# Kernel tuning notes

Measured on AMD Instinct MI355X. Metric: run time of the kernel, lower is better.

## Reference

```python
import jax, jax.numpy as jnp
import numpy as np

B, S, D, H = 4, 2048, 1024, 16
E = D // H  # head_size = 64


def setup_inputs() -> dict:
    key = jax.random.key(0)
    ks = jax.random.split(key, 6)
    scale = 1.0 / np.sqrt(D)
    embedded = jax.random.normal(ks[0], (B, S, D), dtype=jnp.float32)
    # Per-head Q/K/V projection weights, stacked over heads: [H, D, E]
    Wq = jax.random.normal(ks[1], (H, D, E), dtype=jnp.float32) * scale
    Wk = jax.random.normal(ks[2], (H, D, E), dtype=jnp.float32) * scale
    Wv = jax.random.normal(ks[3], (H, D, E), dtype=jnp.float32) * scale
    # Output projection (nn.Linear(model_dim, model_dim))
    Wo = jax.random.normal(ks[4], (D, D), dtype=jnp.float32) * scale
    bo = jax.random.normal(ks[5], (D,), dtype=jnp.float32) * scale
    return {"embedded": embedded, "Wq": Wq, "Wk": Wk, "Wv": Wv, "Wo": Wo, "bo": bo}


def reference(embedded, Wq, Wk, Wv, Wo, bo):
    # Batched over heads instead of the original Python loop; same math.
    q = jnp.einsum('bsd,hde->bhse', embedded, Wq)  # [B,H,S,E]
    k = jnp.einsum('bsd,hde->bhse', embedded, Wk)
    v = jnp.einsum('bsd,hde->bhse', embedded, Wv)
    scores = jnp.einsum('bhse,bhte->bhst', q, k) / jnp.sqrt(jnp.float32(E))
    causal = jnp.tril(jnp.ones((S, S), dtype=bool))  # [S,S]
    scores = jnp.where(causal, scores, jnp.float32(-jnp.inf))
    attn = jax.nn.softmax(scores, axis=-1)  # [B,H,S,S]
    out = jnp.einsum('bhst,bhte->bhse', attn, v)  # [B,H,S,E]
    # concat heads along last dim: [B,S,H*E] == [B,S,D]
    out = out.transpose(0, 2, 1, 3).reshape(B, S, D)
    # output projection (dropout is identity in eval mode)
    return out @ Wo.T + bo
```

## Files before the change

kernel.cpp:

```cpp
#include <hip/hip_runtime.h>
#include <hip/hip_bf16.h>

#define B_ 4
#define S_ 2048
#define D_ 1024
#define H_ 16
#define E_ 64
#define M_ (B_*S_)
#define NQKV_ 3072

typedef __attribute__((ext_vector_type(8))) short bf16x8;
typedef __attribute__((ext_vector_type(4))) float f32x4;
typedef __attribute__((ext_vector_type(16))) float f32x16;
typedef __attribute__((ext_vector_type(4))) unsigned short u16x4;
typedef unsigned short u16;

#define QSCALE 0.18033688011f
#define AS1 __attribute__((address_space(1)))
#define AS3 __attribute__((address_space(3)))

static __device__ __forceinline__ u16 f2bf(float f) {
  unsigned u = __builtin_bit_cast(unsigned, f);
  unsigned r = (u + 0x7FFFu + ((u >> 16) & 1u)) >> 16;
  return (u16)r;
}

static __device__ __forceinline__ unsigned pk2(float a, float b) {
  unsigned r;
  asm("v_cvt_pk_bf16_f32 %0, %1, %2" : "=v"(r) : "v"(a), "v"(b));
  return r;
}


__global__ __launch_bounds__(256) void cvt4(const float* __restrict__ in,
                                            u16* __restrict__ out, int n4) {
  int i = blockIdx.x * 256 + threadIdx.x;
  if (i >= n4) return;
  f32x4 v = ((const f32x4*)in)[i];
  u16x4 o;
  o.x = f2bf(v.x); o.y = f2bf(v.y); o.z = f2bf(v.z); o.w = f2bf(v.w);
  ((u16x4*)out)[i] = o;
}

__global__ __launch_bounds__(256) void cvt_wqkv(const float* __restrict__ Wq,
                                                const float* __restrict__ Wk,
                                                const float* __restrict__ Wv,
                                                u16* __restrict__ Wt) {
  __shared__ float t[64][65];
  const int h = blockIdx.x >> 4;
  const int db = (blockIdx.x & 15) * 64;
  const int tid = threadIdx.x;
  const float* srcs[3] = {Wq, Wk, Wv};
#pragma unroll
  for (int m = 0; m < 3; ++m) {
    const float* src = srcs[m] + (size_t)h * 65536 + (size_t)db * 64;
    __syncthreads();
#pragma unroll
    for (int i = 0; i < 16; ++i) {
      int idx = i * 256 + tid;
      int d = idx >> 6, e = idx & 63;
      t[e][d] = src[d * 64 + e];
    }
    __syncthreads();
    u16* dst = Wt + (size_t)(m * 1024 + h * 64) * 1024 + db;
#pragma unroll
    for (int i = 0; i < 16; ++i) {
      int idx = i * 256 + tid;
      int e = idx >> 6, d = idx & 63;
      dst[(size_t)e * 1024 + d] = f2bf(t[e][d]);
    }
  }
}


template<bool FP32OUT>
__global__ __launch_bounds__(256) void gemm_bt(const u16* __restrict__ A,
                                               const u16* __restrict__ Bt,
                                               void* __restrict__ Cv, int ldC,
                                               u16* __restrict__ Vt,
                                               const float* __restrict__ bias,
                                               int M, int N, int K) {
  __shared__ u16 As[128 * 32];
  __shared__ u16 Bs[128 * 32];
  const int tid = threadIdx.x;
  const int lane = tid & 63, wid = tid >> 6;
  const int bm = blockIdx.x, bn = blockIdx.y;
  const int wr = wid >> 1, wc = wid & 1;
  const int ll = lane & 15, lg = lane >> 4;

  f32x4 acc[4][4] = {};

  const int srow = lane >> 2;
  const int scol = (lane & 3) * 8;

  for (int k0 = 0; k0 < K; k0 += 32) {
#pragma unroll
    for (int p = 0; p < 2; ++p) {
      int row = p * 64 + wid * 16 + srow;
      const u16* ga = A + (size_t)(bm * 128 + row) * K + k0 + scol;
      __builtin_amdgcn_global_load_lds(
          (const AS1 void*)ga, (AS3 void*)(As + p * 2048 + wid * 512), 16, 0, 0);
      const u16* gb = Bt + (size_t)(bn * 128 + row) * K + k0 + scol;
      __builtin_amdgcn_global_load_lds(
          (const AS1 void*)gb, (AS3 void*)(Bs + p * 2048 + wid * 512), 16, 0, 0);
    }
    __syncthreads();
    bf16x8 af[4], bfr[4];
#pragma unroll
    for (int mi = 0; mi < 4; ++mi)
      af[mi] = *(const bf16x8*)&As[(wr * 64 + mi * 16 + ll) * 32 + lg * 8];
#pragma unroll
    for (int ni = 0; ni < 4; ++ni)
      bfr[ni] = *(const bf16x8*)&Bs[(wc * 64 + ni * 16 + ll) * 32 + lg * 8];
#pragma unroll
    for (int mi = 0; mi < 4; ++mi)
#pragma unroll
      for (int ni = 0; ni < 4; ++ni)
        acc[mi][ni] = __builtin_amdgcn_mfma_f32_16x16x32_bf16(af[mi], bfr[ni],
                                                              acc[mi][ni], 0, 0, 0);
    __syncthreads();
  }

  const int crow0 = bm * 128 + wr * 64;
  const int ccol0 = bn * 128 + wc * 64 + ll;
  const bool vblk = (Vt != nullptr) && (bn >= 16);
  const float qs = (Vt != nullptr && bn < 8) ? QSCALE : 1.0f;
  const int sig = (((lg & 1) << 1) | (lg >> 1)) << 2;
#pragma unroll
  for (int mi = 0; mi < 4; ++mi) {
#pragma unroll
    for (int ni = 0; ni < 4; ++ni) {
      int c = ccol0 + ni * 16;
      if (vblk) {
        int r0 = crow0 + mi * 16 + lg * 4;
        int bb = r0 >> 11, s0 = r0 & 2047;
        int s0p = (s0 & ~15) | sig;
        u16x4 pkv;
        pkv.x = f2bf(acc[mi][ni][0]); pkv.y = f2bf(acc[mi][ni][1]);
        pkv.z = f2bf(acc[mi][ni][2]); pkv.w = f2bf(acc[mi][ni][3]);
        *(u16x4*)&Vt[((size_t)(bb * 1024 + (c - 2048))) * 2048 + s0p] = pkv;
      } else {
#pragma unroll
        for (int j = 0; j < 4; ++j) {
          int r = crow0 + mi * 16 + lg * 4 + j;
          if (FP32OUT) {
            ((float*)Cv)[(size_t)r * ldC + c] = acc[mi][ni][j] + bias[c];
          } else {
            ((u16*)Cv)[(size_t)r * ldC + c] = f2bf(acc[mi][ni][j] * qs);
          }
        }
      }
    }
  }
}


#define SWZ(r) ((((r) & 7) ^ ((((r) >> 3) & 3) << 1)) << 4)

__global__ __launch_bounds__(512, 2) void attn(const u16* __restrict__ QK,
                                               const u16* __restrict__ Vt,
                                               u16* __restrict__ AO) {
  __shared__ u16 Klds[4][4096];
  __shared__ u16 Vlds[4][4096];

  const int wg = blockIdx.x;
  const int lin = (wg & 7) * 32 + (wg >> 3);
  const int bh = lin >> 2, pr = lin & 3;
  const int b = bh >> 4, h = bh & 15;
  const int tid = threadIdx.x;
  const int lane = tid & 63, wv = tid >> 6;
  const int lq = lane & 31, hi = lane >> 5;

  const int srow = tid >> 3;
  const int scolb = ((tid & 7) * 16) ^ SWZ(srow);
  const char* ksrc = (const char*)(QK + (size_t)(b * S_ + srow) * 2048 + 1024 + h * E_) + scolb;
  const char* vsrc = (const char*)(Vt + (size_t)(bh * 64 + srow) * 2048) + scolb;

  const int nktA = 4 * pr + 4;
  const int NS = 36;

  auto stage = [&](int sq, int kb) {
    char* kd = (char*)&Klds[0][0] + (sq & 3) * 8192 + wv * 1024;
    char* vd = (char*)&Vlds[0][0] + (sq & 3) * 8192 + wv * 1024;
    __builtin_amdgcn_global_load_lds((const AS1 void*)(ksrc + (size_t)kb * 4096),
                                     (AS3 void*)kd, 16, 0, 0);
    __builtin_amdgcn_global_load_lds((const AS1 void*)(vsrc + kb * 2),
                                     (AS3 void*)vd, 16, 0, 0);
  };

  stage(0, 0);
  stage(1, (1 < nktA ? 1 : 1 - nktA) * 64);

  int seq = 0;
  for (int ph = 0; ph < 2; ++ph) {
    const int qt = ph ? 7 - pr : pr;
    const int nkt = 4 * qt + 4;
    const int qw0 = qt * 256 + wv * 32;
    const int q = qw0 + lq;

    const u16* qp = QK + (size_t)(b * S_ + q) * 2048 + h * E_;
    bf16x8 qf[4];
#pragma unroll
    for (int c = 0; c < 4; ++c)
      qf[c] = *(const bf16x8*)(qp + c * 16 + hi * 8);

    float m_run = -INFINITY, l_part = 0.f;
    f32x16 o0 = {}, o1 = {};

    for (int kt = 0; kt < nkt; ++kt, ++seq) {
      if (seq + 2 < NS) {
        int s2 = seq + 2;
        stage(s2, (s2 < nktA ? s2 : s2 - nktA) * 64);
      }
      if (seq < NS - 2)       asm volatile("s_waitcnt vmcnt(4)" ::: "memory");
      else if (seq == NS - 2) asm volatile("s_waitcnt vmcnt(2)" ::: "memory");
      else                    asm volatile("s_waitcnt vmcnt(0)" ::: "memory");
      __builtin_amdgcn_s_barrier();

      const int kb = kt * 64;
      if (kb > qw0 + 31) continue;
      const char* kbuf = (const char*)&Klds[0][0] + (seq & 3) * 8192;
      const char* vbuf = (const char*)&Vlds[0][0] + (seq & 3) * 8192;

      auto half = [&](int kb2) __attribute__((always_inline)) {
        f32x16 sc = {};
        __builtin_amdgcn_s_setprio(1);
        const int krow = kb2 * 32 + lq;
#pragma unroll
        for (int c = 0; c < 4; ++c) {
          bf16x8 kf = *(const bf16x8*)(kbuf + krow * 128 +
                                       ((c * 32 + hi * 16) ^ SWZ(krow)));
          sc = __builtin_amdgcn_mfma_f32_32x32x16_bf16(kf, qf[c], sc, 0, 0, 0);
        }
        __builtin_amdgcn_s_setprio(0);

        if (kb + kb2 * 32 + 31 > qw0) {
#pragma unroll
          for (int r = 0; r < 16; ++r) {
            int key = kb + kb2 * 32 + (r & 3) + 8 * (r >> 2) + 4 * hi;
            if (key > q) sc[r] = -1e30f;
          }
        }

        float pm = sc[0];
#pragma unroll
        for (int r = 1; r < 16; ++r) pm = fmaxf(pm, sc[r]);
        if (__any(pm - m_run > 8.0f)) {
          float g = fmaxf(pm, __shfl_xor(pm, 32, 64));
          float mn = fmaxf(m_run, g);
          float corr = exp2f(m_run - mn);
          m_run = mn;
          l_part *= corr;
          o0 *= corr;
          o1 *= corr;
        }

        float p[16];
#pragma unroll
        for (int r = 0; r < 16; ++r) {
          p[r] = exp2f(sc[r] - m_run);
          l_part += p[r];
        }
        __builtin_amdgcn_s_setprio(1);
#pragma unroll
        for (int gg = 0; gg < 2; ++gg) {
          union { unsigned w[4]; bf16x8 v; } pf;
          pf.w[0] = pk2(p[gg * 8 + 0], p[gg * 8 + 1]);
          pf.w[1] = pk2(p[gg * 8 + 2], p[gg * 8 + 3]);
          pf.w[2] = pk2(p[gg * 8 + 4], p[gg * 8 + 5]);
          pf.w[3] = pk2(p[gg * 8 + 6], p[gg * 8 + 7]);
          const int g = kb2 * 2 + gg;
          {
            bf16x8 vf = *(const bf16x8*)(vbuf + lq * 128 +
                                         ((g * 32 + hi * 16) ^ SWZ(lq)));
            o0 = __builtin_amdgcn_mfma_f32_32x32x16_bf16(vf, pf.v, o0, 0, 0, 0);
          }
          {
            const int er = 32 + lq;
            bf16x8 vf = *(const bf16x8*)(vbuf + er * 128 +
                                         ((g * 32 + hi * 16) ^ SWZ(er)));
            o1 = __builtin_amdgcn_mfma_f32_32x32x16_bf16(vf, pf.v, o1, 0, 0, 0);
          }
        }
        __builtin_amdgcn_s_setprio(0);
      };

      half(0);
      if (kb + 32 <= qw0 + 31) half(1);
    }

    float l = l_part + __shfl_xor(l_part, 32, 64);
    float rl = 1.0f / l;

#pragma unroll
    for (int qd = 0; qd < 4; ++qd) {
      u16x4 w0, w1;
#pragma unroll
      for (int j = 0; j < 4; ++j) {
        w0[j] = f2bf(o0[qd * 4 + j] * rl);
        w1[j] = f2bf(o1[qd * 4 + j] * rl);
      }
      const size_t base = (size_t)(b * S_ + q) * D_ + h * E_ + 8 * qd + 4 * hi;
      *(u16x4*)&AO[base] = w0;
      *(u16x4*)&AO[base + 32] = w1;
    }
  }
}


extern "C" void kernel_launch(void* const* d_in, const int* in_sizes, int n_in,
                              void* d_out, int out_size, void* d_ws, size_t ws_size,
                              hipStream_t stream) {
  const float* embedded = (const float*)d_in[0];
  const float* Wq = (const float*)d_in[1];
  const float* Wk = (const float*)d_in[2];
  const float* Wv = (const float*)d_in[3];
  const float* Wo = (const float*)d_in[4];
  const float* bo = (const float*)d_in[5];
  float* out = (float*)d_out;

  char* ws = (char*)d_ws;
  u16* X    = (u16*)(ws);
  u16* Wqkv = (u16*)(ws + (16u << 20));
  u16* WoT  = (u16*)(ws + (22u << 20));
  u16* QK   = (u16*)(ws + (24u << 20));
  u16* Vt   = (u16*)(ws + (56u << 20));
  u16* AO   = (u16*)(ws + (72u << 20));

  cvt4<<<8192, 256, 0, stream>>>(embedded, X, 2097152);
  cvt_wqkv<<<256, 256, 0, stream>>>(Wq, Wk, Wv, Wqkv);
  cvt4<<<1024, 256, 0, stream>>>(Wo, WoT, 262144);
  gemm_bt<false><<<dim3(64, 24), 256, 0, stream>>>(X, Wqkv, QK, 2048, Vt,
                                                   nullptr, M_, NQKV_, 1024);
  attn<<<256, 512, 0, stream>>>(QK, Vt, AO);
  gemm_bt<true><<<dim3(64, 8), 256, 0, stream>>>(AO, WoT, out, 1024, nullptr,
                                                 bo, M_, 1024, 1024);
}
```

Baseline: 187.7 us.

## Add dedicated double-buffered QKV GEMM with async global-to-LDS loads

Replaces the generic 128x128 bf16 GEMM for the fused QKV projection with a dedicated 256x192-tile kernel using 512 threads, K-step 64, and double-buffered LDS filled by global_load_lds with an XOR swizzle. The next K-tile is prefetched while the MFMA loop runs, and s_setprio raises priority around the math. This targets the global-load latency exposed by the old single-buffered loop and the low data reuse of its smaller tiles. The cost is far more LDS per block (one block per CU) and a grid of 512 blocks, which may leave load imbalance across CUs.

```diff
diff --git a/kernel.cpp b/kernel.cpp
--- a/kernel.cpp
+++ b/kernel.cpp
@@ -18,6 +18,8 @@
 #define QSCALE 0.18033688011f
 #define AS1 __attribute__((address_space(1)))
 #define AS3 __attribute__((address_space(3)))
+
+#define SWZ(r) ((((r) & 7) ^ ((((r) >> 3) & 3) << 1)) << 4)
 
 static __device__ __forceinline__ u16 f2bf(float f) {
   unsigned u = __builtin_bit_cast(unsigned, f);
@@ -68,6 +70,111 @@
       int idx = i * 256 + tid;
       int e = idx >> 6, d = idx & 63;
       dst[(size_t)e * 1024 + d] = f2bf(t[e][d]);
+    }
+  }
+}
+
+
+__global__ __launch_bounds__(512, 1) void gemm_qkv(const u16* __restrict__ A,
+                                                   const u16* __restrict__ Bt,
+                                                   u16* __restrict__ QK,
+                                                   u16* __restrict__ Vt) {
+  __shared__ u16 As[2][256 * 64];
+  __shared__ u16 Bs[2][192 * 64];
+  const int tid = threadIdx.x;
+  const int lane = tid & 63, wv = tid >> 6;
+  const int ll = lane & 15, lg = lane >> 4;
+  const int wm = wv >> 2, wn = wv & 3;
+  const int bm = blockIdx.x, bn = blockIdx.y;
+
+  const int sr = tid >> 3;
+  const int scb = (tid & 7) * 16;
+  const char* asrc[4];
+  const char* bsrc[3];
+#pragma unroll
+  for (int i = 0; i < 4; ++i) {
+    int row = i * 64 + sr;
+    asrc[i] = (const char*)(A + (size_t)(bm * 256 + row) * 1024) + (scb ^ SWZ(row));
+  }
+#pragma unroll
+  for (int i = 0; i < 3; ++i) {
+    int row = i * 64 + sr;
+    bsrc[i] = (const char*)(Bt + (size_t)(bn * 192 + row) * 1024) + (scb ^ SWZ(row));
+  }
+
+  auto stage = [&](int t) {
+    const size_t adv = (size_t)t * 128;
+    char* ad = (char*)&As[t & 1][0] + tid * 16;
+    char* bd = (char*)&Bs[t & 1][0] + tid * 16;
+#pragma unroll
+    for (int i = 0; i < 4; ++i)
+      __builtin_amdgcn_global_load_lds((const AS1 void*)(asrc[i] + adv),
+                                       (AS3 void*)(ad + i * 8192), 16, 0, 0);
+#pragma unroll
+    for (int i = 0; i < 3; ++i)
+      __builtin_amdgcn_global_load_lds((const AS1 void*)(bsrc[i] + adv),
+                                       (AS3 void*)(bd + i * 8192), 16, 0, 0);
+  };
+
+  f32x4 acc[8][3] = {};
+
+  stage(0);
+  for (int t = 0; t < 16; ++t) {
+    if (t + 1 < 16) stage(t + 1);
+    if (t < 15) asm volatile("s_waitcnt vmcnt(7)" ::: "memory");
+    else        asm volatile("s_waitcnt vmcnt(0)" ::: "memory");
+    __builtin_amdgcn_s_barrier();
+
+    const char* ab = (const char*)&As[t & 1][0];
+    const char* bb = (const char*)&Bs[t & 1][0];
+
+    bf16x8 bf_[3][2];
+#pragma unroll
+    for (int ni = 0; ni < 3; ++ni) {
+      int row = wn * 48 + ni * 16 + ll;
+#pragma unroll
+      for (int ks = 0; ks < 2; ++ks)
+        bf_[ni][ks] = *(const bf16x8*)(bb + row * 128 +
+                                       ((ks * 64 + lg * 16) ^ SWZ(row)));
+    }
+    __builtin_amdgcn_s_setprio(1);
+#pragma unroll
+    for (int mi = 0; mi < 8; ++mi) {
+      int row = wm * 128 + mi * 16 + ll;
+#pragma unroll
+      for (int ks = 0; ks < 2; ++ks) {
+        bf16x8 af = *(const bf16x8*)(ab + row * 128 +
+                                     ((ks * 64 + lg * 16) ^ SWZ(row)));
+#pragma unroll
+        for (int ni = 0; ni < 3; ++ni)
+          acc[mi][ni] = __builtin_amdgcn_mfma_f32_16x16x32_bf16(
+              af, bf_[ni][ks], acc[mi][ni], 0, 0, 0);
+      }
+    }
+    __builtin_amdgcn_s_setprio(0);
+    __builtin_amdgcn_s_barrier();
+  }
+
+  const int sig = (((lg & 1) << 1) | (lg >> 1)) << 2;
+#pragma unroll
+  for (int mi = 0; mi < 8; ++mi) {
+#pragma unroll
+    for (int ni = 0; ni < 3; ++ni) {
+      int c = bn * 192 + wn * 48 + ni * 16 + ll;
+      int r0 = bm * 256 + wm * 128 + mi * 16 + lg * 4;
+      if (c >= 2048) {
+        int bb2 = r0 >> 11, s0 = r0 & 2047;
+        int s0p = (s0 & ~15) | sig;
+        u16x4 pkv;
+        pkv.x = f2bf(acc[mi][ni][0]); pkv.y = f2bf(acc[mi][ni][1]);
+        pkv.z = f2bf(acc[mi][ni][2]); pkv.w = f2bf(acc[mi][ni][3]);
+        *(u16x4*)&Vt[((size_t)(bb2 * 1024 + (c - 2048))) * 2048 + s0p] = pkv;
+      } else {
+        const float qs = (c < 1024) ? QSCALE : 1.0f;
+#pragma unroll
+        for (int j = 0; j < 4; ++j)
+          QK[(size_t)(r0 + j) * 2048 + c] = f2bf(acc[mi][ni][j] * qs);
+      }
     }
   }
 }
@@ -123,39 +230,24 @@
 
   const int crow0 = bm * 128 + wr * 64;
   const int ccol0 = bn * 128 + wc * 64 + ll;
-  const bool vblk = (Vt != nullptr) && (bn >= 16);
-  const float qs = (Vt != nullptr && bn < 8) ? QSCALE : 1.0f;
-  const int sig = (((lg & 1) << 1) | (lg >> 1)) << 2;
 #pragma unroll
   for (int mi = 0; mi < 4; ++mi) {
 #pragma unroll
     for (int ni = 0; ni < 4; ++ni) {
       int c = ccol0 + ni * 16;
-      if (vblk) {
-        int r0 = crow0 + mi * 16 + lg * 4;
-        int bb = r0 >> 11, s0 = r0 & 2047;
-        int s0p = (s0 & ~15) | sig;
-        u16x4 pkv;
-        pkv.x = f2bf(acc[mi][ni][0]); pkv.y = f2bf(acc[mi][ni][1]);
-        pkv.z = f2bf(acc[mi][ni][2]); pkv.w = f2bf(acc[mi][ni][3]);
-        *(u16x4*)&Vt[((size_t)(bb * 1024 + (c - 2048))) * 2048 + s0p] = pkv;
-      } else {
-#pragma unroll
-        for (int j = 0; j < 4; ++j) {
-          int r = crow0 + mi * 16 + lg * 4 + j;
-          if (FP32OUT) {
-            ((float*)Cv)[(size_t)r * ldC + c] = acc[mi][ni][j] + bias[c];
-          } else {
-            ((u16*)Cv)[(size_t)r * ldC + c] = f2bf(acc[mi][ni][j] * qs);
-          }
+#pragma unroll
+      for (int j = 0; j < 4; ++j) {
+        int r = crow0 + mi * 16 + lg * 4 + j;
+        if (FP32OUT) {
+          ((float*)Cv)[(size_t)r * ldC + c] = acc[mi][ni][j] + bias[c];
+        } else {
+          ((u16*)Cv)[(size_t)r * ldC + c] = f2bf(acc[mi][ni][j]);
         }
       }
     }
   }
 }
 
-
-#define SWZ(r) ((((r) & 7) ^ ((((r) >> 3) & 3) << 1)) << 4)
 
 __global__ __launch_bounds__(512, 2) void attn(const u16* __restrict__ QK,
                                                const u16* __restrict__ Vt,
@@ -330,8 +422,7 @@
   cvt4<<<8192, 256, 0, stream>>>(embedded, X, 2097152);
   cvt_wqkv<<<256, 256, 0, stream>>>(Wq, Wk, Wv, Wqkv);
   cvt4<<<1024, 256, 0, stream>>>(Wo, WoT, 262144);
-  gemm_bt<false><<<dim3(64, 24), 256, 0, stream>>>(X, Wqkv, QK, 2048, Vt,
-                                                   nullptr, M_, NQKV_, 1024);
+  gemm_qkv<<<dim3(32, 16), 512, 0, stream>>>(X, Wqkv, QK, Vt);
   attn<<<256, 512, 0, stream>>>(QK, Vt, AO);
   gemm_bt<true><<<dim3(64, 8), 256, 0, stream>>>(AO, WoT, out, 1024, nullptr,
                                                  bo, M_, 1024, 1024);
```

Result: faster. 179.9 us (-4.2%).

## Fuse conversion kernels and rewrite GEMMs with larger tiles and triple-buffered LDS pipeline

Applied to the files above, without the earlier changes.

The three fp32-to-bf16 conversion launches are merged into one kernel that dispatches on block index. Both projection GEMMs are rewritten as 512-thread kernels with larger tiles (256x384 for QKV, 256x128 for the output). They use a three-stage global-to-LDS prefetch with explicit vmcnt waits and raised scheduling priority around the MFMA loop. The goal is to cut launch overhead and hide global load latency behind compute. The cost is more LDS and registers per block and fewer blocks (256 per GEMM), which can hurt occupancy and load balance.

```diff
diff --git a/kernel.cpp b/kernel.cpp
--- a/kernel.cpp
+++ b/kernel.cpp
@@ -19,6 +19,8 @@
 #define AS1 __attribute__((address_space(1)))
 #define AS3 __attribute__((address_space(3)))
 
+#define SWZ(r) ((((r) & 7) ^ ((((r) >> 3) & 3) << 1)) << 4)
+
 static __device__ __forceinline__ u16 f2bf(float f) {
   unsigned u = __builtin_bit_cast(unsigned, f);
   unsigned r = (u + 0x7FFFu + ((u >> 16) & 1u)) >> 16;
@@ -32,130 +34,232 @@
 }
 
 
-__global__ __launch_bounds__(256) void cvt4(const float* __restrict__ in,
-                                            u16* __restrict__ out, int n4) {
-  int i = blockIdx.x * 256 + threadIdx.x;
-  if (i >= n4) return;
-  f32x4 v = ((const f32x4*)in)[i];
-  u16x4 o;
-  o.x = f2bf(v.x); o.y = f2bf(v.y); o.z = f2bf(v.z); o.w = f2bf(v.w);
-  ((u16x4*)out)[i] = o;
-}
-
-__global__ __launch_bounds__(256) void cvt_wqkv(const float* __restrict__ Wq,
-                                                const float* __restrict__ Wk,
-                                                const float* __restrict__ Wv,
-                                                u16* __restrict__ Wt) {
+__global__ __launch_bounds__(256) void cvt_fused(const float* __restrict__ emb,
+                                                 const float* __restrict__ Wo,
+                                                 const float* __restrict__ Wq,
+                                                 const float* __restrict__ Wk,
+                                                 const float* __restrict__ Wv,
+                                                 u16* __restrict__ X,
+                                                 u16* __restrict__ WoT,
+                                                 u16* __restrict__ Wt) {
   __shared__ float t[64][65];
-  const int h = blockIdx.x >> 4;
-  const int db = (blockIdx.x & 15) * 64;
+  const int bid = blockIdx.x;
   const int tid = threadIdx.x;
-  const float* srcs[3] = {Wq, Wk, Wv};
-#pragma unroll
-  for (int m = 0; m < 3; ++m) {
-    const float* src = srcs[m] + (size_t)h * 65536 + (size_t)db * 64;
-    __syncthreads();
-#pragma unroll
-    for (int i = 0; i < 16; ++i) {
-      int idx = i * 256 + tid;
-      int d = idx >> 6, e = idx & 63;
-      t[e][d] = src[d * 64 + e];
-    }
-    __syncthreads();
-    u16* dst = Wt + (size_t)(m * 1024 + h * 64) * 1024 + db;
-#pragma unroll
-    for (int i = 0; i < 16; ++i) {
-      int idx = i * 256 + tid;
-      int e = idx >> 6, d = idx & 63;
-      dst[(size_t)e * 1024 + d] = f2bf(t[e][d]);
-    }
-  }
-}
-
-
-template<bool FP32OUT>
-__global__ __launch_bounds__(256) void gemm_bt(const u16* __restrict__ A,
-                                               const u16* __restrict__ Bt,
-                                               void* __restrict__ Cv, int ldC,
-                                               u16* __restrict__ Vt,
-                                               const float* __restrict__ bias,
-                                               int M, int N, int K) {
-  __shared__ u16 As[128 * 32];
-  __shared__ u16 Bs[128 * 32];
+  if (bid < 8192) {
+    int i = bid * 256 + tid;
+    f32x4 v = ((const f32x4*)emb)[i];
+    u16x4 o;
+    o.x = f2bf(v.x); o.y = f2bf(v.y); o.z = f2bf(v.z); o.w = f2bf(v.w);
+    ((u16x4*)X)[i] = o;
+  } else if (bid < 9216) {
+    int i = (bid - 8192) * 256 + tid;
+    f32x4 v = ((const f32x4*)Wo)[i];
+    u16x4 o;
+    o.x = f2bf(v.x); o.y = f2bf(v.y); o.z = f2bf(v.z); o.w = f2bf(v.w);
+    ((u16x4*)WoT)[i] = o;
+  } else {
+    const int blk = bid - 9216;
+    const int h = blk >> 4;
+    const int db = (blk & 15) * 64;
+    const float* srcs[3] = {Wq, Wk, Wv};
+#pragma unroll
+    for (int m = 0; m < 3; ++m) {
+      const float* src = srcs[m] + (size_t)h * 65536 + (size_t)db * 64;
+      __syncthreads();
+#pragma unroll
+      for (int i = 0; i < 16; ++i) {
+        int idx = i * 256 + tid;
+        int d = idx >> 6, e = idx & 63;
+        t[e][d] = src[d * 64 + e];
+      }
+      __syncthreads();
+      u16* dst = Wt + (size_t)(m * 1024 + h * 64) * 1024 + db;
+#pragma unroll
+      for (int i = 0; i < 16; ++i) {
+        int idx = i * 256 + tid;
+        int e = idx >> 6, d = idx & 63;
+        dst[(size_t)e * 1024 + d] = f2bf(t[e][d]);
+      }
+    }
+  }
+}
+
+
+__global__ __launch_bounds__(512, 2) void gemm_qkv(const u16* __restrict__ A,
+                                                   const u16* __restrict__ Bt,
+                                                   u16* __restrict__ QK,
+                                                   u16* __restrict__ Vt) {
+  __shared__ u16 As[3][256 * 32];
+  __shared__ u16 Bs[3][384 * 32];
   const int tid = threadIdx.x;
-  const int lane = tid & 63, wid = tid >> 6;
+  const int lane = tid & 63, wv = tid >> 6;
+  const int ll = lane & 15, lg = lane >> 4;
+  const int wm = wv >> 2, wn = wv & 3;
   const int bm = blockIdx.x, bn = blockIdx.y;
-  const int wr = wid >> 1, wc = wid & 1;
-  const int ll = lane & 15, lg = lane >> 4;
-
-  f32x4 acc[4][4] = {};
-
-  const int srow = lane >> 2;
-  const int scol = (lane & 3) * 8;
-
-  for (int k0 = 0; k0 < K; k0 += 32) {
-#pragma unroll
-    for (int p = 0; p < 2; ++p) {
-      int row = p * 64 + wid * 16 + srow;
-      const u16* ga = A + (size_t)(bm * 128 + row) * K + k0 + scol;
-      __builtin_amdgcn_global_load_lds(
-          (const AS1 void*)ga, (AS3 void*)(As + p * 2048 + wid * 512), 16, 0, 0);
-      const u16* gb = Bt + (size_t)(bn * 128 + row) * K + k0 + scol;
-      __builtin_amdgcn_global_load_lds(
-          (const AS1 void*)gb, (AS3 void*)(Bs + p * 2048 + wid * 512), 16, 0, 0);
-    }
-    __syncthreads();
-    bf16x8 af[4], bfr[4];
-#pragma unroll
-    for (int mi = 0; mi < 4; ++mi)
-      af[mi] = *(const bf16x8*)&As[(wr * 64 + mi * 16 + ll) * 32 + lg * 8];
-#pragma unroll
-    for (int ni = 0; ni < 4; ++ni)
-      bfr[ni] = *(const bf16x8*)&Bs[(wc * 64 + ni * 16 + ll) * 32 + lg * 8];
-#pragma unroll
-    for (int mi = 0; mi < 4; ++mi)
-#pragma unroll
-      for (int ni = 0; ni < 4; ++ni)
-        acc[mi][ni] = __builtin_amdgcn_mfma_f32_16x16x32_bf16(af[mi], bfr[ni],
-                                                              acc[mi][ni], 0, 0, 0);
-    __syncthreads();
-  }
-
-  const int crow0 = bm * 128 + wr * 64;
-  const int ccol0 = bn * 128 + wc * 64 + ll;
-  const bool vblk = (Vt != nullptr) && (bn >= 16);
-  const float qs = (Vt != nullptr && bn < 8) ? QSCALE : 1.0f;
+
+  const int sr = tid >> 2;
+  const int scb = (tid & 3) * 16;
+  const char* a0 = (const char*)(A + (size_t)(bm * 256 + sr) * 1024) + scb;
+  const char* a1 = (const char*)(A + (size_t)(bm * 256 + 128 + sr) * 1024) + scb;
+  const char* b0 = (const char*)(Bt + (size_t)(bn * 384 + sr) * 1024) + scb;
+  const char* b1 = (const char*)(Bt + (size_t)(bn * 384 + 128 + sr) * 1024) + scb;
+  const char* b2 = (const char*)(Bt + (size_t)(bn * 384 + 256 + sr) * 1024) + scb;
+
+  auto stage = [&](int t, int bi) {
+    const size_t adv = (size_t)t * 64;
+    char* ad = (char*)&As[bi][0] + tid * 16;
+    char* bd = (char*)&Bs[bi][0] + tid * 16;
+    __builtin_amdgcn_global_load_lds((const AS1 void*)(a0 + adv), (AS3 void*)ad, 16, 0, 0);
+    __builtin_amdgcn_global_load_lds((const AS1 void*)(a1 + adv), (AS3 void*)(ad + 8192), 16, 0, 0);
+    __builtin_amdgcn_global_load_lds((const AS1 void*)(b0 + adv), (AS3 void*)bd, 16, 0, 0);
+    __builtin_amdgcn_global_load_lds((const AS1 void*)(b1 + adv), (AS3 void*)(bd + 8192), 16, 0, 0);
+    __builtin_amdgcn_global_load_lds((const AS1 void*)(b2 + adv), (AS3 void*)(bd + 16384), 16, 0, 0);
+  };
+
+  f32x4 acc[8][6] = {};
+
+  stage(0, 0);
+  stage(1, 1);
+  for (int t = 0; t < 32; ++t) {
+    const int cur = t % 3;
+    if (t + 2 < 32) {
+      stage(t + 2, (t + 2) % 3);
+      asm volatile("s_waitcnt vmcnt(10)" ::: "memory");
+    } else if (t + 1 < 32) {
+      asm volatile("s_waitcnt vmcnt(5)" ::: "memory");
+    } else {
+      asm volatile("s_waitcnt vmcnt(0)" ::: "memory");
+    }
+    __builtin_amdgcn_s_barrier();
+
+    const char* ab = (const char*)&As[cur][0];
+    const char* bb = (const char*)&Bs[cur][0];
+
+    bf16x8 bf[6];
+#pragma unroll
+    for (int ni = 0; ni < 6; ++ni) {
+      int row = wn * 96 + ni * 16 + ll;
+      bf[ni] = *(const bf16x8*)(bb + row * 64 + lg * 16);
+    }
+    __builtin_amdgcn_s_setprio(1);
+#pragma unroll
+    for (int mi = 0; mi < 8; ++mi) {
+      int row = wm * 128 + mi * 16 + ll;
+      bf16x8 af = *(const bf16x8*)(ab + row * 64 + lg * 16);
+#pragma unroll
+      for (int ni = 0; ni < 6; ++ni)
+        acc[mi][ni] = __builtin_amdgcn_mfma_f32_16x16x32_bf16(
+            af, bf[ni], acc[mi][ni], 0, 0, 0);
+    }
+    __builtin_amdgcn_s_setprio(0);
+    __builtin_amdgcn_s_barrier();
+  }
+
   const int sig = (((lg & 1) << 1) | (lg >> 1)) << 2;
 #pragma unroll
-  for (int mi = 0; mi < 4; ++mi) {
-#pragma unroll
-    for (int ni = 0; ni < 4; ++ni) {
-      int c = ccol0 + ni * 16;
-      if (vblk) {
-        int r0 = crow0 + mi * 16 + lg * 4;
-        int bb = r0 >> 11, s0 = r0 & 2047;
+  for (int mi = 0; mi < 8; ++mi) {
+#pragma unroll
+    for (int ni = 0; ni < 6; ++ni) {
+      int c = bn * 384 + wn * 96 + ni * 16 + ll;
+      int r0 = bm * 256 + wm * 128 + mi * 16 + lg * 4;
+      if (c >= 2048) {
+        int bb2 = r0 >> 11, s0 = r0 & 2047;
         int s0p = (s0 & ~15) | sig;
         u16x4 pkv;
         pkv.x = f2bf(acc[mi][ni][0]); pkv.y = f2bf(acc[mi][ni][1]);
         pkv.z = f2bf(acc[mi][ni][2]); pkv.w = f2bf(acc[mi][ni][3]);
-        *(u16x4*)&Vt[((size_t)(bb * 1024 + (c - 2048))) * 2048 + s0p] = pkv;
+        *(u16x4*)&Vt[((size_t)(bb2 * 1024 + (c - 2048))) * 2048 + s0p] = pkv;
       } else {
-#pragma unroll
-        for (int j = 0; j < 4; ++j) {
-          int r = crow0 + mi * 16 + lg * 4 + j;
-          if (FP32OUT) {
-            ((float*)Cv)[(size_t)r * ldC + c] = acc[mi][ni][j] + bias[c];
-          } else {
-            ((u16*)Cv)[(size_t)r * ldC + c] = f2bf(acc[mi][ni][j] * qs);
-          }
-        }
+        const float qs = (c < 1024) ? QSCALE : 1.0f;
+#pragma unroll
+        for (int j = 0; j < 4; ++j)
+          QK[(size_t)(r0 + j) * 2048 + c] = f2bf(acc[mi][ni][j] * qs);
       }
     }
   }
 }
 
 
-#define SWZ(r) ((((r) & 7) ^ ((((r) >> 3) & 3) << 1)) << 4)
+__global__ __launch_bounds__(512, 2) void gemm_out(const u16* __restrict__ A,
+                                                   const u16* __restrict__ Bt,
+                                                   float* __restrict__ C,
+                                                   const float* __restrict__ bias) {
+  __shared__ u16 As[3][256 * 32];
+  __shared__ u16 Bs[3][128 * 32];
+  const int tid = threadIdx.x;
+  const int lane = tid & 63, wv = tid >> 6;
+  const int ll = lane & 15, lg = lane >> 4;
+  const int wm = wv >> 2, wn = wv & 3;
+  const int bm = blockIdx.x, bn = blockIdx.y;
+
+  const int sr = tid >> 2;
+  const int scb = (tid & 3) * 16;
+  const char* a0 = (const char*)(A + (size_t)(bm * 256 + sr) * 1024) + scb;
+  const char* a1 = (const char*)(A + (size_t)(bm * 256 + 128 + sr) * 1024) + scb;
+  const char* b0 = (const char*)(Bt + (size_t)(bn * 128 + sr) * 1024) + scb;
+
+  auto stage = [&](int t, int bi) {
+    const size_t adv = (size_t)t * 64;
+    char* ad = (char*)&As[bi][0] + tid * 16;
+    char* bd = (char*)&Bs[bi][0] + tid * 16;
+    __builtin_amdgcn_global_load_lds((const AS1 void*)(a0 + adv), (AS3 void*)ad, 16, 0, 0);
+    __builtin_amdgcn_global_load_lds((const AS1 void*)(a1 + adv), (AS3 void*)(ad + 8192), 16, 0, 0);
+    __builtin_amdgcn_global_load_lds((const AS1 void*)(b0 + adv), (AS3 void*)bd, 16, 0, 0);
+  };
+
+  f32x4 acc[8][2] = {};
+
+  stage(0, 0);
+  stage(1, 1);
+  for (int t = 0; t < 32; ++t) {
+    const int cur = t % 3;
+    if (t + 2 < 32) {
+      stage(t + 2, (t + 2) % 3);
+      asm volatile("s_waitcnt vmcnt(6)" ::: "memory");
+    } else if (t + 1 < 32) {
+      asm volatile("s_waitcnt vmcnt(3)" ::: "memory");
+    } else {
+      asm volatile("s_waitcnt vmcnt(0)" ::: "memory");
+    }
+    __builtin_amdgcn_s_barrier();
+
+    const char* ab = (const char*)&As[cur][0];
+    const char* bb = (const char*)&Bs[cur][0];
+
+    bf16x8 bf[2];
+#pragma unroll
+    for (int ni = 0; ni < 2; ++ni) {
+      int row = wn * 32 + ni * 16 + ll;
+      bf[ni] = *(const bf16x8*)(bb + row * 64 + lg * 16);
+    }
+    __builtin_amdgcn_s_setprio(1);
+#pragma unroll
+    for (int mi = 0; mi < 8; ++mi) {
+      int row = wm * 128 + mi * 16 + ll;
+      bf16x8 af = *(const bf16x8*)(ab + row * 64 + lg * 16);
+#pragma unroll
+      for (int ni = 0; ni < 2; ++ni)
+        acc[mi][ni] = __builtin_amdgcn_mfma_f32_16x16x32_bf16(
+            af, bf[ni], acc[mi][ni], 0, 0, 0);
+    }
+    __builtin_amdgcn_s_setprio(0);
+    __builtin_amdgcn_s_barrier();
+  }
+
+#pragma unroll
+  for (int mi = 0; mi < 8; ++mi) {
+#pragma unroll
+    for (int ni = 0; ni < 2; ++ni) {
+      int c = bn * 128 + wn * 32 + ni * 16 + ll;
+      int r0 = bm * 256 + wm * 128 + mi * 16 + lg * 4;
+      float bv = bias[c];
+#pragma unroll
+      for (int j = 0; j < 4; ++j)
+        C[(size_t)(r0 + j) * 1024 + c] = acc[mi][ni][j] + bv;
+    }
+  }
+}
+
 
 __global__ __launch_bounds__(512, 2) void attn(const u16* __restrict__ QK,
                                                const u16* __restrict__ Vt,
@@ -327,12 +431,8 @@
   u16* Vt   = (u16*)(ws + (56u << 20));
   u16* AO   = (u16*)(ws + (72u << 20));
 
-  cvt4<<<8192, 256, 0, stream>>>(embedded, X, 2097152);
-  cvt_wqkv<<<256, 256, 0, stream>>>(Wq, Wk, Wv, Wqkv);
-  cvt4<<<1024, 256, 0, stream>>>(Wo, WoT, 262144);
-  gemm_bt<false><<<dim3(64, 24), 256, 0, stream>>>(X, Wqkv, QK, 2048, Vt,
-                                                   nullptr, M_, NQKV_, 1024);
+  cvt_fused<<<9472, 256, 0, stream>>>(embedded, Wo, Wq, Wk, Wv, X, WoT, Wqkv);
+  gemm_qkv<<<dim3(32, 8), 512, 0, stream>>>(X, Wqkv, QK, Vt);
   attn<<<256, 512, 0, stream>>>(QK, Vt, AO);
-  gemm_bt<true><<<dim3(64, 8), 256, 0, stream>>>(AO, WoT, out, 1024, nullptr,
-                                                 bo, M_, 1024, 1024);
-}
+  gemm_out<<<dim3(32, 8), 512, 0, stream>>>(AO, WoT, out, bo);
+}
```

Measured after the change: 181.0 us. -3.6%, faster.
